# Performance work log

Measured on AMD Instinct MI355X. Metric: run time of the kernel, lower is better.

Reference implementation:

```python
import jax, jax.numpy as jnp
import numpy as np

B = 16384      # batch of states
N = 64         # neighbors per state -> x width = 5 + 2*N = 133
H = 128        # embed / hidden feature dim (num_inputs)
HID = 256      # actor/critic hidden size
OUT = 2        # action dim


def setup_inputs() -> dict:
    key = jax.random.key(0)
    ks = jax.random.split(key, 12)
    w = lambda k, shp: (jax.random.normal(k, shp, jnp.float32) * 0.1)
    b = lambda n: jnp.full((n,), 0.1, jnp.float32)
    return {
        "x": jax.random.normal(ks[0], (B, 5 + 2 * N), jnp.float32),
        # embbedLayer: Linear(2,128)
        "We": w(ks[1], (H, 2)), "be": b(H),
        # hlayer: Linear(128,128)
        "Wh": w(ks[2], (H, H)), "bh": b(H),
        # attentionLayer: Linear(256,1)
        "Wa": w(ks[3], (1, 2 * H)), "ba": b(1),
        # layer2: Linear(133,128)
        "W2": w(ks[4], (H, H + 5)), "b2": b(H),
        # critic: Linear(128,256) -> Linear(256,1)
        "Wc1": w(ks[5], (HID, H)), "bc1": b(HID),
        "Wc2": w(ks[6], (1, HID)), "bc2": b(1),
        # actor: Linear(128,256) -> Linear(256,2)
        "Wp1": w(ks[7], (HID, H)), "bp1": b(HID),
        "Wp2": w(ks[8], (OUT, HID)), "bp2": b(OUT),
        # log_std parameter (std=0.0 -> ones*0.0)
        "log_std": jnp.zeros((1, OUT), jnp.float32),
    }


def reference(x, We, be, Wh, bh, Wa, ba, W2, b2,
              Wc1, bc1, Wc2, bc2, Wp1, bp1, Wp2, bp2, log_std):
    Bn = x.shape[0]
    state_loc = x[:, :5]                       # [B,5]
    nb = x[:, 5:].reshape(Bn, -1, 2)           # [B,N,2] ragged loop flattened

    e = jax.nn.relu(jnp.einsum('bnd,hd->bnh', nb, We) + be)   # [B,N,H]
    em = jnp.mean(e, axis=1, keepdims=True)                    # [B,1,H]
    h = jax.nn.relu(jnp.einsum('bnh,oh->bno', e, Wh) + bh)     # [B,N,H]

    # attentionLayer(hstack(e, em)): split Wa into e-part and mean-part
    Wa_e, Wa_m = Wa[:, :H], Wa[:, H:]
    score = jax.nn.relu(
        jnp.einsum('bnh,oh->bno', e, Wa_e)
        + jnp.einsum('bkh,oh->bko', em, Wa_m)   # [B,1,1] broadcasts over N
        + ba
    )                                            # [B,N,1]
    attn = jax.nn.softmax(score, axis=1)         # softmax over neighbors
    mean_feature = jnp.mean(attn * h, axis=1)    # [B,H]

    t = jax.nn.relu(
        jnp.concatenate([state_loc, mean_feature], axis=1) @ W2.T + b2
    )                                            # [B,H]

    value = jax.nn.relu(t @ Wc1.T + bc1) @ Wc2.T + bc2   # [B,1]
    mu = jax.nn.relu(t @ Wp1.T + bp1) @ Wp2.T + bp2       # [B,2]
    std = jnp.broadcast_to(jnp.exp(log_std), mu.shape)    # [B,2]
    return mu, std, value
```

## Files before the change

kernel.cpp:

```cpp
#include <hip/hip_runtime.h>

#define BATCH 16384
#define XDIM  133
#define RPB   2
#define EROW  272
#define MB    64
#define CROW  336
#define TROW  272

#define WH_OFF   0
#define W2_OFF   16384
#define WC1_OFF  36864
#define WP1_OFF  69632
#define WA_OFF   102400
#define WE2_OFF  102528
#define MFG_OFF  208896

typedef __attribute__((ext_vector_type(8))) _Float16 half8;
typedef __attribute__((ext_vector_type(4))) _Float16 half4v;
typedef __attribute__((ext_vector_type(2))) _Float16 half2v;
typedef __attribute__((ext_vector_type(4))) float    f32x4;
typedef __attribute__((ext_vector_type(4))) unsigned int uint4v;

__device__ __forceinline__ float relu(float v) { return fmaxf(v, 0.f); }
__device__ __forceinline__ unsigned short f2h(float f) {
    _Float16 h = (_Float16)f;
    return __builtin_bit_cast(unsigned short, h);
}
__device__ __forceinline__ half2v pk2h(float a, float b) {
    return __builtin_bit_cast(half2v, __builtin_amdgcn_cvt_pkrtz(a, b));
}

__global__ __launch_bounds__(256)
void ac_prep(const float* __restrict__ Wh, const float* __restrict__ W2,
             const float* __restrict__ Wc1, const float* __restrict__ Wp1,
             const float* __restrict__ Wa, const float* __restrict__ We,
             const float* __restrict__ be, unsigned short* __restrict__ wsH)
{
    const int idx = blockIdx.x * 256 + threadIdx.x;
    const int stride = gridDim.x * 256;
    for (int i = idx; i < 128*128; i += stride) wsH[WH_OFF + i] = f2h(Wh[i]);
    for (int i = idx; i < 128*160; i += stride) {
        int o = i / 160, ck = i - o*160;
        float w = (ck < 128) ? W2[o*XDIM + 5 + ck]
                             : ((ck < 133) ? W2[o*XDIM + (ck - 128)] : 0.f);
        wsH[W2_OFF + i] = f2h(w);
    }
    for (int i = idx; i < 256*128; i += stride) wsH[WC1_OFF + i] = f2h(Wc1[i]);
    for (int i = idx; i < 256*128; i += stride) wsH[WP1_OFF + i] = f2h(Wp1[i]);
    for (int i = idx; i < 128;     i += stride) wsH[WA_OFF  + i] = f2h(Wa[i]);
    for (int hp = idx; hp < 128;   hp += stride) {
        wsH[WE2_OFF + hp*8 + 0] = f2h(We[4*hp+0]);
        wsH[WE2_OFF + hp*8 + 1] = f2h(We[4*hp+2]);
        wsH[WE2_OFF + hp*8 + 2] = f2h(We[4*hp+1]);
        wsH[WE2_OFF + hp*8 + 3] = f2h(We[4*hp+3]);
        wsH[WE2_OFF + hp*8 + 4] = f2h(be[2*hp+0]);
        wsH[WE2_OFF + hp*8 + 5] = f2h(be[2*hp+1]);
        wsH[WE2_OFF + hp*8 + 6] = f2h(Wa[128+2*hp+0]);
        wsH[WE2_OFF + hp*8 + 7] = f2h(Wa[128+2*hp+1]);
    }
}

__global__ __launch_bounds__(256, 4)
void ac_attn(const float* __restrict__ x,
             const float* __restrict__ bh,  const float* __restrict__ ba,
             const unsigned short* __restrict__ wsH,
             char* __restrict__ mfG)
{
    __shared__ __align__(16) char  eH[RPB * 64 * EROW];
    __shared__ __align__(16) char  xsH[RPB * 64 * 8];
    __shared__ __align__(16) float attnS[RPB][64];
    __shared__ __align__(16) float mfS[RPB][128];
    __shared__ __align__(16) float pS[4][64];
    __shared__            float cpart[4][RPB];

    const int tid  = threadIdx.x;
    const int lane = tid & 63;
    const int wave = tid >> 6;
    const int b0   = blockIdx.x * RPB;

    if (tid < 128) {
        int r = tid >> 6, n = tid & 63;
        float2 nb = *(const float2*)(x + (size_t)(b0 + r) * XDIM + 5 + 2*n);
        half2v s0 = pk2h(nb.x, nb.x);
        half2v s1 = pk2h(nb.y, nb.y);
        half4v s; s[0] = s0[0]; s[1] = s0[1]; s[2] = s1[0]; s[3] = s1[1];
        *(half4v*)(xsH + (r*64 + n)*8) = s;
    }
    __syncthreads();

    {
        const int hp = lane;
        const int q  = wave;
        half8 wp = *(const half8*)(wsH + WE2_OFF + hp*8);
        half2v W0 = {wp[0], wp[1]};
        half2v W1 = {wp[2], wp[3]};
        half2v BE = {wp[4], wp[5]};
        half2v WAM = {wp[6], wp[7]};
        const half2v Z = {(_Float16)0.0f, (_Float16)0.0f};
        #pragma unroll
        for (int r = 0; r < RPB; ++r) {
            float ca = 0.f;
            #pragma unroll
            for (int i = 0; i < 16; ++i) {
                int n = q*16 + i;
                half4v s = *(const half4v*)(xsH + (r*64 + n)*8);
                half2v s0 = {s[0], s[1]};
                half2v s1 = {s[2], s[3]};
                half2v X = s0*W0 + BE;
                X = s1*W1 + X;
                X = __builtin_elementwise_max(X, Z);
                ca = __builtin_amdgcn_fdot2(X, WAM, ca, false);
                *(half2v*)(eH + (r*64 + n)*EROW + (hp << 2)) = X;
            }
            #pragma unroll
            for (int off = 1; off < 64; off <<= 1) ca += __shfl_xor(ca, off);
            if (lane == 0) cpart[wave][r] = ca;
        }
    }
    __syncthreads();

    {
        const int r  = wave & 1;
        const int kh = wave >> 1;
        const int n  = lane;
        const int row = r*64 + n;
        const half2v* wa = (const half2v*)(wsH + WA_OFF) + kh*32;
        float s = 0.f;
        #pragma unroll
        for (int k16 = 0; k16 < 8; ++k16) {
            half8 v = *(const half8*)(eH + row*EROW + kh*128 + k16*16);
            const half2v* v2 = (const half2v*)&v;
            #pragma unroll
            for (int j = 0; j < 4; ++j)
                s = __builtin_amdgcn_fdot2(v2[j], wa[k16*4 + j], s, false);
        }
        pS[wave][n] = s;
    }
    __syncthreads();

    if (wave < RPB) {
        const int r = wave;
        const int n = lane;
        float s = pS[r][n] + pS[2 + r][n];
        float c = (cpart[0][r] + cpart[1][r] + cpart[2][r] + cpart[3][r]) * (1.f/64.f) + ba[0];
        float sc = relu(s + c);
        float m = sc;
        #pragma unroll
        for (int off = 1; off < 64; off <<= 1) m = fmaxf(m, __shfl_xor(m, off));
        float p = __expf(sc - m);
        float sum = p;
        #pragma unroll
        for (int off = 1; off < 64; off <<= 1) sum += __shfl_xor(sum, off);
        attnS[r][n] = p / (sum * 64.f);
    }
    __syncthreads();

    {
        const int lo = lane & 15;
        const int g  = lane >> 4;
        const int c0 = wave*32 + lo;
        const int c1 = c0 + 16;
        const unsigned short* WhH = wsH + WH_OFF;
        half8 bfr[2][4];
        #pragma unroll
        for (int kk = 0; kk < 4; ++kk) {
            int kb = kk*32 + g*8;
            bfr[0][kk] = *(const half8*)(WhH + c0*128 + kb);
            bfr[1][kk] = *(const half8*)(WhH + c1*128 + kb);
        }
        const float bh0 = bh[c0], bh1 = bh[c1];

        #pragma unroll
        for (int r = 0; r < RPB; ++r) {
            float mf0 = 0.f, mf1 = 0.f;
            #pragma unroll
            for (int nt = 0; nt < 4; ++nt) {
                const int arow = r*64 + nt*16 + lo;
                half8 af[4];
                #pragma unroll
                for (int kk = 0; kk < 4; ++kk)
                    af[kk] = *(const half8*)(eH + arow*EROW + kk*64 + g*16);
                f32x4 acc0 = {0.f, 0.f, 0.f, 0.f};
                f32x4 acc1 = {0.f, 0.f, 0.f, 0.f};
                #pragma unroll
                for (int kk = 0; kk < 4; ++kk) {
                    acc0 = __builtin_amdgcn_mfma_f32_16x16x32_f16(af[kk], bfr[0][kk], acc0, 0, 0, 0);
                    acc1 = __builtin_amdgcn_mfma_f32_16x16x32_f16(af[kk], bfr[1][kk], acc1, 0, 0, 0);
                }
                f32x4 at4 = *(const f32x4*)&attnS[r][nt*16 + g*4];
                #pragma unroll
                for (int j = 0; j < 4; ++j) {
                    mf0 = fmaf(at4[j], relu(acc0[j] + bh0), mf0);
                    mf1 = fmaf(at4[j], relu(acc1[j] + bh1), mf1);
                }
            }
            mf0 += __shfl_xor(mf0, 16);  mf0 += __shfl_xor(mf0, 32);
            mf1 += __shfl_xor(mf1, 16);  mf1 += __shfl_xor(mf1, 32);
            if (lane < 16) {
                mfS[r][wave*32 + lane]      = mf0;
                mfS[r][wave*32 + 16 + lane] = mf1;
            }
        }
    }
    __syncthreads();

    if (tid < RPB * 64) {
        int r = tid >> 6, c = tid & 63;
        *(half2v*)(mfG + ((size_t)(b0 + r) * 128 + 2*c) * 2) = pk2h(mfS[r][2*c], mfS[r][2*c+1]);
    }
}

__global__ __launch_bounds__(256, 1)
void ac_heads(const float* __restrict__ x, const char* __restrict__ mfG,
              const unsigned short* __restrict__ wsH,
              const float* __restrict__ b2,
              const float* __restrict__ bc1, const float* __restrict__ Wc2,
              const float* __restrict__ bc2,
              const float* __restrict__ bp1, const float* __restrict__ Wp2,
              const float* __restrict__ bp2,
              const float* __restrict__ log_std,
              float* __restrict__ out)
{
    __shared__ __align__(16) char catS[MB * CROW];
    __shared__ __align__(16) char tS[MB * TROW];
    __shared__ float redV [2][MB];
    __shared__ float redM0[2][MB];
    __shared__ float redM1[2][MB];

    const int tid  = threadIdx.x;
    const int lane = tid & 63;
    const int wave = tid >> 6;
    const int lo   = lane & 15;
    const int g    = lane >> 4;
    const int b0   = blockIdx.x * MB;

    for (int i = tid * 16; i < MB * CROW; i += 256 * 16)
        *(uint4v*)(catS + i) = (uint4v){0, 0, 0, 0};
    __syncthreads();
    for (int c = tid; c < MB * 16; c += 256) {
        int row = c >> 4, sl = c & 15;
        uint4v v = *(const uint4v*)(mfG + (size_t)(b0 + row) * 256 + sl * 16);
        *(uint4v*)(catS + row * CROW + sl * 16) = v;
    }
    for (int m = tid; m < MB; m += 256) {
        const float* xr = x + (size_t)(b0 + m) * XDIM;
        #pragma unroll
        for (int k = 0; k < 5; ++k)
            *(unsigned short*)(catS + m * CROW + 256 + 2*k) = f2h(xr[k]);
    }
    __syncthreads();

    {
        const int o = wave * 32 + lo;
        const unsigned short* W2H = wsH + W2_OFF;
        half8 bw[2][5];
        #pragma unroll
        for (int nt2 = 0; nt2 < 2; ++nt2)
            #pragma unroll
            for (int kk = 0; kk < 5; ++kk)
                bw[nt2][kk] = *(const half8*)(W2H + (size_t)(o + nt2*16)*160 + kk*32 + g*8);
        const float bb0 = b2[o], bb1 = b2[o + 16];
        #pragma unroll
        for (int mt = 0; mt < 4; ++mt) {
            const int arow = mt*16 + lo;
            half8 af[5];
            #pragma unroll
            for (int kk = 0; kk < 5; ++kk)
                af[kk] = *(const half8*)(catS + arow*CROW + kk*64 + g*16);
            f32x4 a0 = {0.f,0.f,0.f,0.f}, a1 = {0.f,0.f,0.f,0.f};
            #pragma unroll
            for (int kk = 0; kk < 5; ++kk) {
                a0 = __builtin_amdgcn_mfma_f32_16x16x32_f16(af[kk], bw[0][kk], a0, 0, 0, 0);
                a1 = __builtin_amdgcn_mfma_f32_16x16x32_f16(af[kk], bw[1][kk], a1, 0, 0, 0);
            }
            #pragma unroll
            for (int j = 0; j < 4; ++j) {
                int m = mt*16 + g*4 + j;
                *(unsigned short*)(tS + m*TROW + o*2)      = f2h(relu(a0[j] + bb0));
                *(unsigned short*)(tS + m*TROW + (o+16)*2) = f2h(relu(a1[j] + bb1));
            }
        }
    }
    __syncthreads();

    {
        const bool isval = (wave < 2);
        const unsigned short* W1H = wsH + (isval ? WC1_OFF : WP1_OFF);
        const float* bb = isval ? bc1 : bp1;
        const int obase = (wave & 1) * 128;
        float sA[4][4], sB[4][4];
        #pragma unroll
        for (int mt = 0; mt < 4; ++mt)
            #pragma unroll
            for (int j = 0; j < 4; ++j) { sA[mt][j] = 0.f; sB[mt][j] = 0.f; }

        #pragma unroll
        for (int np = 0; np < 4; ++np) {
            const int oA = obase + np*32 + lo;
            const int oB = oA + 16;
            half8 bf0[4], bf1[4];
            #pragma unroll
            for (int kk = 0; kk < 4; ++kk) {
                bf0[kk] = *(const half8*)(W1H + (size_t)oA*128 + kk*32 + g*8);
                bf1[kk] = *(const half8*)(W1H + (size_t)oB*128 + kk*32 + g*8);
            }
            const float biasA = bb[oA], biasB = bb[oB];
            float wA0, wB0, wA1 = 0.f, wB1 = 0.f;
            if (isval) { wA0 = Wc2[oA]; wB0 = Wc2[oB]; }
            else       { wA0 = Wp2[oA]; wB0 = Wp2[oB]; wA1 = Wp2[256+oA]; wB1 = Wp2[256+oB]; }

            #pragma unroll
            for (int mt = 0; mt < 4; ++mt) {
                const int arow = mt*16 + lo;
                half8 af[4];
                #pragma unroll
                for (int kk = 0; kk < 4; ++kk)
                    af[kk] = *(const half8*)(tS + arow*TROW + kk*64 + g*16);
                f32x4 a0 = {0.f,0.f,0.f,0.f}, a1 = {0.f,0.f,0.f,0.f};
                #pragma unroll
                for (int kk = 0; kk < 4; ++kk) {
                    a0 = __builtin_amdgcn_mfma_f32_16x16x32_f16(af[kk], bf0[kk], a0, 0, 0, 0);
                    a1 = __builtin_amdgcn_mfma_f32_16x16x32_f16(af[kk], bf1[kk], a1, 0, 0, 0);
                }
                #pragma unroll
                for (int j = 0; j < 4; ++j) {
                    float uA = relu(a0[j] + biasA);
                    float uB = relu(a1[j] + biasB);
                    sA[mt][j] += wA0*uA + wB0*uB;
                    sB[mt][j] += wA1*uA + wB1*uB;
                }
            }
        }
        #pragma unroll
        for (int mt = 0; mt < 4; ++mt)
            #pragma unroll
            for (int j = 0; j < 4; ++j) {
                #pragma unroll
                for (int off = 1; off < 16; off <<= 1) {
                    sA[mt][j] += __shfl_xor(sA[mt][j], off);
                    sB[mt][j] += __shfl_xor(sB[mt][j], off);
                }
            }
        if (lo == 0) {
            #pragma unroll
            for (int mt = 0; mt < 4; ++mt)
                #pragma unroll
                for (int j = 0; j < 4; ++j) {
                    int m = mt*16 + g*4 + j;
                    if (isval) redV[wave][m] = sA[mt][j];
                    else { redM0[wave-2][m] = sA[mt][j]; redM1[wave-2][m] = sB[mt][j]; }
                }
        }
    }
    __syncthreads();

    if (tid < MB) {
        const int m = tid;
        const int b = b0 + m;
        out[b*2 + 0]           = redM0[0][m] + redM0[1][m] + bp2[0];
        out[b*2 + 1]           = redM1[0][m] + redM1[1][m] + bp2[1];
        out[2*BATCH + b*2 + 0] = expf(log_std[0]);
        out[2*BATCH + b*2 + 1] = expf(log_std[1]);
        out[4*BATCH + b]       = redV[0][m] + redV[1][m] + bc2[0];
    }
}

extern "C" void kernel_launch(void* const* d_in, const int* in_sizes, int n_in,
                              void* d_out, int out_size, void* d_ws, size_t ws_size,
                              hipStream_t stream) {
    (void)in_sizes; (void)n_in; (void)ws_size; (void)out_size;
    const float* x       = (const float*)d_in[0];
    const float* We      = (const float*)d_in[1];
    const float* be      = (const float*)d_in[2];
    const float* Wh      = (const float*)d_in[3];
    const float* bh      = (const float*)d_in[4];
    const float* Wa      = (const float*)d_in[5];
    const float* ba      = (const float*)d_in[6];
    const float* W2      = (const float*)d_in[7];
    const float* b2      = (const float*)d_in[8];
    const float* Wc1     = (const float*)d_in[9];
    const float* bc1     = (const float*)d_in[10];
    const float* Wc2     = (const float*)d_in[11];
    const float* bc2     = (const float*)d_in[12];
    const float* Wp1     = (const float*)d_in[13];
    const float* bp1     = (const float*)d_in[14];
    const float* Wp2     = (const float*)d_in[15];
    const float* bp2     = (const float*)d_in[16];
    const float* log_std = (const float*)d_in[17];

    unsigned short* wsH = (unsigned short*)d_ws;
    char* mfG = (char*)d_ws + MFG_OFF;

    hipLaunchKernelGGL(ac_prep, dim3(64), dim3(256), 0, stream,
                       Wh, W2, Wc1, Wp1, Wa, We, be, wsH);
    hipLaunchKernelGGL(ac_attn, dim3(BATCH / RPB), dim3(256), 0, stream,
                       x, bh, ba, wsH, mfG);
    hipLaunchKernelGGL(ac_heads, dim3(BATCH / MB), dim3(256), 0, stream,
                       x, mfG, wsH, b2, bc1, Wc2, bc2, bp1, Wp2, bp2,
                       log_std, (float*)d_out);
}
```

Measured before the change: 80.48 us.

## Fuse attention scoring, softmax and weighted sum per wave to drop barriers

```diff
diff --git a/kernel.cpp b/kernel.cpp
--- a/kernel.cpp
+++ b/kernel.cpp
@@ -69,9 +69,6 @@
 {
     __shared__ __align__(16) char  eH[RPB * 64 * EROW];
     __shared__ __align__(16) char  xsH[RPB * 64 * 8];
-    __shared__ __align__(16) float attnS[RPB][64];
-    __shared__ __align__(16) float mfS[RPB][128];
-    __shared__ __align__(16) float pS[4][64];
     __shared__            float cpart[4][RPB];
 
     const int tid  = threadIdx.x;
@@ -121,30 +118,27 @@
     __syncthreads();
 
     {
-        const int r  = wave & 1;
-        const int kh = wave >> 1;
-        const int n  = lane;
-        const int row = r*64 + n;
-        const half2v* wa = (const half2v*)(wsH + WA_OFF) + kh*32;
+        const int lo = lane & 15;
+        const int g  = lane >> 4;
+        const int r  = wave >> 1;
+        const int ch = wave & 1;
+
         float s = 0.f;
-        #pragma unroll
-        for (int k16 = 0; k16 < 8; ++k16) {
-            half8 v = *(const half8*)(eH + row*EROW + kh*128 + k16*16);
-            const half2v* v2 = (const half2v*)&v;
-            #pragma unroll
-            for (int j = 0; j < 4; ++j)
-                s = __builtin_amdgcn_fdot2(v2[j], wa[k16*4 + j], s, false);
-        }
-        pS[wave][n] = s;
-    }
-    __syncthreads();
-
-    if (wave < RPB) {
-        const int r = wave;
-        const int n = lane;
-        float s = pS[r][n] + pS[2 + r][n];
-        float c = (cpart[0][r] + cpart[1][r] + cpart[2][r] + cpart[3][r]) * (1.f/64.f) + ba[0];
-        float sc = relu(s + c);
+        {
+            const int row = r*64 + lane;
+            const half2v* wa = (const half2v*)(wsH + WA_OFF);
+            #pragma unroll
+            for (int k16 = 0; k16 < 16; ++k16) {
+                half8 v = *(const half8*)(eH + row*EROW + k16*16);
+                const half2v* v2 = (const half2v*)&v;
+                #pragma unroll
+                for (int j = 0; j < 4; ++j)
+                    s = __builtin_amdgcn_fdot2(v2[j], wa[k16*4 + j], s, false);
+            }
+        }
+        const float cterm = (cpart[0][r] + cpart[1][r] + cpart[2][r] + cpart[3][r])
+                            * (1.f/64.f) + ba[0];
+        float sc = relu(s + cterm);
         float m = sc;
         #pragma unroll
         for (int off = 1; off < 64; off <<= 1) m = fmaxf(m, __shfl_xor(m, off));
@@ -152,27 +146,20 @@
         float sum = p;
         #pragma unroll
         for (int off = 1; off < 64; off <<= 1) sum += __shfl_xor(sum, off);
-        attnS[r][n] = p / (sum * 64.f);
-    }
-    __syncthreads();
-
-    {
-        const int lo = lane & 15;
-        const int g  = lane >> 4;
-        const int c0 = wave*32 + lo;
-        const int c1 = c0 + 16;
+        const float attn = p / (sum * 64.f);
+
         const unsigned short* WhH = wsH + WH_OFF;
-        half8 bfr[2][4];
-        #pragma unroll
-        for (int kk = 0; kk < 4; ++kk) {
-            int kb = kk*32 + g*8;
-            bfr[0][kk] = *(const half8*)(WhH + c0*128 + kb);
-            bfr[1][kk] = *(const half8*)(WhH + c1*128 + kb);
-        }
-        const float bh0 = bh[c0], bh1 = bh[c1];
-
-        #pragma unroll
-        for (int r = 0; r < RPB; ++r) {
+        #pragma unroll
+        for (int cp = 0; cp < 2; ++cp) {
+            const int c0 = ch*64 + cp*32 + lo;
+            const int c1 = c0 + 16;
+            half8 bfr[2][4];
+            #pragma unroll
+            for (int kk = 0; kk < 4; ++kk) {
+                bfr[0][kk] = *(const half8*)(WhH + (size_t)c0*128 + kk*32 + g*8);
+                bfr[1][kk] = *(const half8*)(WhH + (size_t)c1*128 + kk*32 + g*8);
+            }
+            const float bh0 = bh[c0], bh1 = bh[c1];
             float mf0 = 0.f, mf1 = 0.f;
             #pragma unroll
             for (int nt = 0; nt < 4; ++nt) {
@@ -181,33 +168,31 @@
                 #pragma unroll
                 for (int kk = 0; kk < 4; ++kk)
                     af[kk] = *(const half8*)(eH + arow*EROW + kk*64 + g*16);
-                f32x4 acc0 = {0.f, 0.f, 0.f, 0.f};
-                f32x4 acc1 = {0.f, 0.f, 0.f, 0.f};
+                f32x4 acc0 = {0.f,0.f,0.f,0.f};
+                f32x4 acc1 = {0.f,0.f,0.f,0.f};
                 #pragma unroll
                 for (int kk = 0; kk < 4; ++kk) {
                     acc0 = __builtin_amdgcn_mfma_f32_16x16x32_f16(af[kk], bfr[0][kk], acc0, 0, 0, 0);
                     acc1 = __builtin_amdgcn_mfma_f32_16x16x32_f16(af[kk], bfr[1][kk], acc1, 0, 0, 0);
                 }
-                f32x4 at4 = *(const f32x4*)&attnS[r][nt*16 + g*4];
+                float at[4];
+                #pragma unroll
+                for (int j = 0; j < 4; ++j)
+                    at[j] = __shfl(attn, nt*16 + g*4 + j);
                 #pragma unroll
                 for (int j = 0; j < 4; ++j) {
-                    mf0 = fmaf(at4[j], relu(acc0[j] + bh0), mf0);
-                    mf1 = fmaf(at4[j], relu(acc1[j] + bh1), mf1);
+                    mf0 = fmaf(at[j], relu(acc0[j] + bh0), mf0);
+                    mf1 = fmaf(at[j], relu(acc1[j] + bh1), mf1);
                 }
             }
             mf0 += __shfl_xor(mf0, 16);  mf0 += __shfl_xor(mf0, 32);
             mf1 += __shfl_xor(mf1, 16);  mf1 += __shfl_xor(mf1, 32);
             if (lane < 16) {
-                mfS[r][wave*32 + lane]      = mf0;
-                mfS[r][wave*32 + 16 + lane] = mf1;
-            }
-        }
-    }
-    __syncthreads();
-
-    if (tid < RPB * 64) {
-        int r = tid >> 6, c = tid & 63;
-        *(half2v*)(mfG + ((size_t)(b0 + r) * 128 + 2*c) * 2) = pk2h(mfS[r][2*c], mfS[r][2*c+1]);
+                size_t base = (size_t)(b0 + r)*128 + ch*64 + cp*32 + lane;
+                *(unsigned short*)(mfG + base*2)        = f2h(mf0);
+                *(unsigned short*)(mfG + (base + 16)*2) = f2h(mf1);
+            }
+        }
     }
 }
 
```

After: 95.68 us. 18.9% more time.
